# Optimization experiments

Measured on AMD Instinct MI355X. Metric: run time of the kernel, lower is better.

The kernel has to match this reference:

```python
import jax, jax.numpy as jnp
import numpy as np

D_INPUT, D_MODEL, D_OUTPUT, D_STATE, FACTOR = 100, 256, 100, 64, 2
N2 = D_STATE // 2  # complex conjugate-pair states (S4D)
B_SZ, L_SEQ = 16, 4096


def setup_inputs() -> dict:
    key = jax.random.key(0)
    ks = jax.random.split(key, 12)
    H, N = D_MODEL, N2
    # S4D ('diag-lin', zoh, real_transform='exp') parameters
    log_dt = jax.random.uniform(ks[0], (H,)) * (np.log(0.1) - np.log(0.001)) + np.log(0.001)
    log_A_real = jnp.log(0.5 * jnp.ones((H, N), jnp.float32))
    A_imag = jnp.pi * jnp.broadcast_to(jnp.arange(N, dtype=jnp.float32), (H, N))
    B_re = jnp.ones((H, N), jnp.float32)
    B_im = jnp.zeros((H, N), jnp.float32)
    C_re = jax.random.normal(ks[1], (H, N), jnp.float32)
    C_im = jax.random.normal(ks[2], (H, N), jnp.float32)
    Dskip = jax.random.normal(ks[3], (H,), jnp.float32)
    return {
        'x': jax.random.normal(ks[4], (B_SZ, L_SEQ, D_INPUT), jnp.float32),
        'enc_w': jax.random.normal(ks[5], (D_MODEL, D_INPUT), jnp.float32) / np.sqrt(D_INPUT),
        'enc_b': jnp.zeros((D_MODEL,), jnp.float32),
        'log_dt': log_dt, 'log_A_real': log_A_real, 'A_imag': A_imag,
        'B_re': B_re, 'B_im': B_im, 'C_re': C_re, 'C_im': C_im, 'Dskip': Dskip,
        'ln_g': jnp.ones((D_MODEL,), jnp.float32),
        'ln_b': jnp.zeros((D_MODEL,), jnp.float32),
        'dec1_w': jax.random.normal(ks[6], (D_MODEL * FACTOR, D_MODEL), jnp.float32) / np.sqrt(D_MODEL),
        'dec1_b': jnp.zeros((D_MODEL * FACTOR,), jnp.float32),
        'dec2_w': jax.random.normal(ks[7], (D_OUTPUT, D_MODEL * FACTOR), jnp.float32) / np.sqrt(D_MODEL * FACTOR),
        'dec2_b': jnp.zeros((D_OUTPUT,), jnp.float32),
    }


def s4d_kernel(log_dt, log_A_real, A_imag, B_re, B_im, C_re, C_im, L):
    # diagonal SSM kernel, ZOH discretization: K[h,l] = 2 Re sum_n C'_hn exp(dt_h A_hn)^l
    dt = jnp.exp(log_dt)[:, None]                      # (H,1)
    A = -jnp.exp(log_A_real) + 1j * A_imag             # (H,N)
    C = (B_re + 1j * B_im) * (C_re + 1j * C_im)        # (H,N), B folded into C
    dtA = dt * A                                       # (H,N)
    C = C * (jnp.exp(dtA) - 1.0) / A                   # ZOH correction
    V = jnp.exp(dtA[:, :, None] * jnp.arange(L))       # (H,N,L) Vandermonde
    return 2.0 * jnp.einsum('hn,hnl->hl', C, V).real   # (H,L)


def reference(x, enc_w, enc_b, log_dt, log_A_real, A_imag, B_re, B_im, C_re, C_im,
              Dskip, ln_g, ln_b, dec1_w, dec1_b, dec2_w, dec2_b):
    B, L, _ = x.shape
    u = (x @ enc_w.T + enc_b).transpose(0, 2, 1)       # (B,H,L)
    # FFTConv (single layer), dropout = identity (eval)
    k = s4d_kernel(log_dt, log_A_real, A_imag, B_re, B_im, C_re, C_im, L)
    n = 2 * L
    y = jnp.fft.irfft(jnp.fft.rfft(u, n=n) * jnp.fft.rfft(k, n=n)[None], n=n)[..., :L]
    y = y + u * Dskip[None, :, None]
    y = jax.nn.gelu(y, approximate=False)
    h = y + u                                          # residual
    # LayerNorm over channel dim
    t = h.transpose(0, 2, 1)                           # (B,L,H)
    mu = t.mean(-1, keepdims=True)
    var = jnp.mean((t - mu) ** 2, axis=-1, keepdims=True)
    t = (t - mu) / jnp.sqrt(var + 1e-5) * ln_g + ln_b
    # decoder MLP
    out = jax.nn.gelu(t @ dec1_w.T + dec1_b, approximate=False) @ dec2_w.T + dec2_b
    return out
```

## Files before the change

kernel.cpp:

```cpp
#include <hip/hip_runtime.h>
#include <hip/hip_bf16.h>

#define BB    16
#define LL    4096
#define DIN   100
#define HD    256
#define NN    32
#define DHID  512
#define DOUT  100
#define MROWS (BB*LL)
#define CH    64
#define CC    64
#define NCH   (BB*CC)

#define OFF_WRE    0
#define OFF_WIM    8192
#define OFF_KRE    16384
#define OFF_KIM    24576
#define OFF_WCHR   32768
#define OFF_WCHI   40960
#define OFF_ENCB   49152
#define OFF_DSK    49408
#define OFF_LNG    49664
#define OFF_LNB    49920
#define OFF_B1     50176
#define OFF_B2     50688
#define OFF_WENCB  50816
#define OFF_W1B    67200
#define OFF_W2B    132736
#define OFF_WFL    165504
#define OFF_BY     1230464
#define OFF_VST    2279040
#define OFF_UH     2803328
#define OFF_S      11191936
#define OFF_YH     19580544
#define OFF_TB     OFF_S
#define OFF_XB     OFF_YH

typedef __bf16 bf16x8 __attribute__((ext_vector_type(8)));
typedef float  f32x4  __attribute__((ext_vector_type(4)));

static __device__ __forceinline__ int probe_bf16(const void* lng) {
    return ((const unsigned int*)lng)[0] != 0x3f800000u;
}
static __device__ __forceinline__ float ldin(const void* p, long i, int isbf) {
    return isbf ? __bfloat162float(((const __hip_bfloat16*)p)[i]) : ((const float*)p)[i];
}
static __device__ __forceinline__ unsigned short f2bf(float v) {
    union { float f; unsigned u; } c; c.f = v;
    unsigned r = c.u + 0x7fffu + ((c.u >> 16) & 1u);
    return (unsigned short)(r >> 16);
}
static __device__ __forceinline__ float bf2f(unsigned short v) {
    union { unsigned u; float f; } c; c.u = ((unsigned)v) << 16; return c.f;
}
static __device__ __forceinline__ float gelu_f(float x) {
    float z  = fabsf(x) * 0.70710678118654752f;
    float tt = __builtin_amdgcn_rcpf(fmaf(0.3275911f, z, 1.0f));
    float p  = tt * fmaf(tt, fmaf(tt, fmaf(tt, fmaf(tt, 1.061405429f, -1.453152027f),
                          1.421413741f), -0.284496736f), 0.254829592f);
    float er = 1.0f - p * __expf(-z * z);
    return 0.5f * x * (1.0f + copysignf(er, x));
}
static __device__ __forceinline__ void gl2lds16(const unsigned short* g, unsigned short* l) {
    __builtin_amdgcn_global_load_lds(
        (const __attribute__((address_space(1))) unsigned int*)g,
        (__attribute__((address_space(3))) unsigned int*)l, 16, 0, 0);
}

__global__ __launch_bounds__(256) void k_prep(
    const void* encw, const void* encb, const void* logdt, const void* loga,
    const void* aim, const void* bre, const void* bim, const void* cre,
    const void* cim, const void* dsk, const void* lng, const void* lnb,
    const void* w1, const void* b1, const void* w2, const void* b2, float* ws)
{
    const int isbf = probe_bf16(lng);
    unsigned short* WEB = (unsigned short*)(ws + OFF_WENCB);
    unsigned short* W1B = (unsigned short*)(ws + OFF_W1B);
    unsigned short* W2B = (unsigned short*)(ws + OFF_W2B);
    const int total = 8192 + 256*4 + 512 + 128 + 32768 + 131072 + 65536;
    for (int idx = blockIdx.x * blockDim.x + threadIdx.x; idx < total;
         idx += gridDim.x * blockDim.x) {
        int i = idx;
        if (i < 8192) {
            int h = i >> 5;
            float dt  = expf(ldin(logdt, h, isbf));
            float Are = -expf(ldin(loga, i, isbf));
            float Aim = ldin(aim, i, isbf);
            float er  = expf(dt * Are);
            float sv, cv; sincosf(dt * Aim, &sv, &cv);
            float wre = er * cv, wim = er * sv;
            float Bre = ldin(bre, i, isbf), Bim = ldin(bim, i, isbf);
            float Cre = ldin(cre, i, isbf), Cim = ldin(cim, i, isbf);
            float C0re = Bre*Cre - Bim*Cim;
            float C0im = Bre*Cim + Bim*Cre;
            float inv = 1.0f / (Are*Are + Aim*Aim);
            float nre = wre - 1.0f, nim = wim;
            float Zre = (nre*Are + nim*Aim) * inv;
            float Zim = (nim*Are - nre*Aim) * inv;
            float kre = 2.0f * (C0re*Zre - C0im*Zim);
            float kim = -2.0f * (C0re*Zim + C0im*Zre);
            ws[OFF_WRE + i] = wre;  ws[OFF_WIM + i] = wim;
            ws[OFF_KRE + i] = kre;  ws[OFF_KIM + i] = kim;
            float* Wf = ws + OFF_WFL + (long)h * 4160 + 2*(i & 31);
            float pr = 1.0f, pi = 0.0f;
            for (int d = 0; d <= 64; ++d) {
                Wf[d*64]     = pr;
                Wf[d*64 + 1] = pi;
                float tr = pr*wre - pi*wim;
                pi = pr*wim + pi*wre; pr = tr;
            }
            ws[OFF_WCHR + i] = Wf[64*64];
            ws[OFF_WCHI + i] = Wf[64*64 + 1];
        } else if ((i -= 8192) < 256) {
            ws[OFF_ENCB + i] = ldin(encb, i, isbf);
        } else if ((i -= 256) < 256) {
            ws[OFF_DSK + i] = ldin(dsk, i, isbf);
        } else if ((i -= 256) < 256) {
            ws[OFF_LNG + i] = ldin(lng, i, isbf);
        } else if ((i -= 256) < 256) {
            ws[OFF_LNB + i] = ldin(lnb, i, isbf);
        } else if ((i -= 256) < 512) {
            ws[OFF_B1 + i] = ldin(b1, i, isbf);
        } else if ((i -= 512) < 128) {
            ws[OFF_B2 + i] = (i < 100) ? ldin(b2, i, isbf) : 0.0f;
        } else if ((i -= 128) < 32768) {
            int h = i >> 7, k = i & 127;
            WEB[i] = (k < 100) ? f2bf(ldin(encw, (long)h*100 + k, isbf)) : (unsigned short)0;
        } else if ((i -= 32768) < 131072) {
            W1B[i] = f2bf(ldin(w1, i, isbf));
        } else if ((i -= 131072) < 65536) {
            int j = i >> 9, k = i & 511;
            W2B[i] = (j < 100) ? f2bf(ldin(w2, (long)j*512 + k, isbf)) : (unsigned short)0;
        }
    }
}

__global__ __launch_bounds__(256) void k_xcvt(const void* x, const void* lng, float* ws)
{
    const int isbf = probe_bf16(lng);
    unsigned short* Xb = (unsigned short*)(ws + OFF_XB);
    const int total = 65536 * 16;
    for (int s = blockIdx.x * 256 + threadIdx.x; s < total; s += 1024 * 256) {
        int row = s >> 4, slot = s & 15;
        int k0 = slot * 8;
        unsigned short pk[8];
        if (!isbf) {
            const float* xr = (const float*)x + (long)row * 100;
            if (slot < 12) {
                float4 a = *(const float4*)(xr + k0);
                float4 b = *(const float4*)(xr + k0 + 4);
                pk[0]=f2bf(a.x); pk[1]=f2bf(a.y); pk[2]=f2bf(a.z); pk[3]=f2bf(a.w);
                pk[4]=f2bf(b.x); pk[5]=f2bf(b.y); pk[6]=f2bf(b.z); pk[7]=f2bf(b.w);
            } else if (slot == 12) {
                float4 a = *(const float4*)(xr + 96);
                pk[0]=f2bf(a.x); pk[1]=f2bf(a.y); pk[2]=f2bf(a.z); pk[3]=f2bf(a.w);
                pk[4]=0; pk[5]=0; pk[6]=0; pk[7]=0;
            } else {
                #pragma unroll
                for (int j = 0; j < 8; ++j) pk[j] = 0;
            }
        } else {
            const unsigned short* xr = (const unsigned short*)x + (long)row * 100;
            if (slot < 12) {
                *(uint2*)&pk[0] = *(const uint2*)(xr + k0);
                *(uint2*)&pk[4] = *(const uint2*)(xr + k0 + 4);
            } else if (slot == 12) {
                *(uint2*)&pk[0] = *(const uint2*)(xr + 96);
                pk[4]=0; pk[5]=0; pk[6]=0; pk[7]=0;
            } else {
                #pragma unroll
                for (int j = 0; j < 8; ++j) pk[j] = 0;
            }
        }
        *(float4*)&Xb[(long)row * 128 + k0] = *(const float4*)pk;
    }
}

__global__ __launch_bounds__(256) void k_tker(float* ws)
{
    __shared__ float Wp[65*65];
    __shared__ float kr[32], ki[32], Ks[64];
    int h = blockIdx.x;
    int t = threadIdx.x;
    for (int idx = t; idx < 4160; idx += 256) {
        int d = idx >> 6, c = idx & 63;
        Wp[d*65 + c] = ws[OFF_WFL + (long)h*4160 + idx];
    }
    if (t < 32) kr[t] = ws[OFF_KRE + h*32 + t];
    else if (t < 64) ki[t-32] = ws[OFF_KIM + h*32 + (t-32)];
    __syncthreads();
    if (t < 64) {
        float s = 0.0f;
        #pragma unroll
        for (int n = 0; n < 32; ++n)
            s += kr[n]*Wp[t*65 + 2*n] + ki[n]*Wp[t*65 + 2*n + 1];
        Ks[t] = s;
    }
    __syncthreads();
    unsigned short* BY = (unsigned short*)(ws + OFF_BY) + (long)h*8192;
    for (int idx = t; idx < 8192; idx += 256) {
        int j = idx >> 7, k = idx & 127;
        float v;
        if (k < 64) {
            v = (k <= j) ? Ks[j - k] : 0.0f;
        } else {
            int c = k - 64, n = c >> 1;
            float pr = Wp[(j+1)*65 + 2*n], pi = Wp[(j+1)*65 + 2*n + 1];
            v = ((c & 1) == 0) ? (kr[n]*pr + ki[n]*pi) : (ki[n]*pr - kr[n]*pi);
        }
        BY[idx] = f2bf(v);
    }
    unsigned short* Vst = (unsigned short*)(ws + OFF_VST) + (long)h*4096;
    for (int idx = t; idx < 4096; idx += 256) {
        int comp = idx >> 6, i = idx & 63;
        Vst[idx] = f2bf(Wp[(63 - i)*65 + comp]);
    }
}

__global__ __launch_bounds__(256) void k_encm(float* ws)
{
    __shared__ unsigned short SM[32768];
    unsigned short* Cs = SM;
    const unsigned short* Xb  = (const unsigned short*)(ws + OFF_XB);
    const unsigned short* WEB = (const unsigned short*)(ws + OFF_WENCB);
    int bid = blockIdx.x;
    int rt = bid >> 1, ct = bid & 1;
    long row0 = (long)rt * 128;
    int c0 = ct * 128;
    int t = threadIdx.x;
    int lane = t & 63, wv = t >> 6;
    int wm = (wv & 1) * 64, wn = (wv >> 1) * 64;
    int quad = lane >> 4, mr = lane & 15;
    int swz = lane & 7;
    int sr = t >> 3, sdst = (t & 7) * 8, ssrc = ((t & 7) ^ (sr & 7)) * 8;
    f32x4 acc[4][4] = {};
    #pragma unroll
    for (int it = 0; it < 4; ++it) {
        int r = sr + it * 32;
        gl2lds16(&Xb[(row0 + r) * 128 + ssrc], &SM[r * 64 + sdst]);
        gl2lds16(&WEB[(long)(c0 + r) * 128 + ssrc], &SM[8192 + r * 64 + sdst]);
    }
    __syncthreads();
    #pragma unroll
    for (int kc = 0; kc < 2; ++kc) {
        const unsigned short* As = &SM[(kc & 1) * 16384];
        const unsigned short* Bs = As + 8192;
        if (kc == 0) {
            #pragma unroll
            for (int it = 0; it < 4; ++it) {
                int r = sr + it * 32;
                gl2lds16(&Xb[(row0 + r) * 128 + 64 + ssrc], &SM[16384 + r * 64 + sdst]);
                gl2lds16(&WEB[(long)(c0 + r) * 128 + 64 + ssrc], &SM[24576 + r * 64 + sdst]);
            }
        }
        #pragma unroll
        for (int ks = 0; ks < 64; ks += 32) {
            int co = (((ks >> 3) | quad) ^ swz) * 8;
            bf16x8 af[4], bfr[4];
            #pragma unroll
            for (int i = 0; i < 4; ++i)
                af[i] = *(const bf16x8*)&As[(wm + i*16 + mr)*64 + co];
            #pragma unroll
            for (int j = 0; j < 4; ++j)
                bfr[j] = *(const bf16x8*)&Bs[(wn + j*16 + mr)*64 + co];
            #pragma unroll
            for (int i = 0; i < 4; ++i)
                #pragma unroll
                for (int j = 0; j < 4; ++j)
                    acc[i][j] = __builtin_amdgcn_mfma_f32_16x16x32_bf16(af[i], bfr[j], acc[i][j], 0, 0, 0);
        }
        __syncthreads();
    }
    const float* eb = ws + OFF_ENCB;
    #pragma unroll
    for (int j = 0; j < 4; ++j) {
        int hloc = wn + j*16 + mr;
        float bb = eb[c0 + hloc];
        #pragma unroll
        for (int i = 0; i < 4; ++i) {
            int l0 = wm + i*16 + quad*4;
            unsigned short pk[4];
            #pragma unroll
            for (int reg = 0; reg < 4; ++reg)
                pk[reg] = f2bf(acc[i][j][reg] + bb);
            *(uint2*)&Cs[hloc*136 + l0] = *(uint2*)pk;
        }
    }
    __syncthreads();
    unsigned short* Uh = (unsigned short*)(ws + OFF_UH);
    #pragma unroll
    for (int it = 0; it < 8; ++it) {
        int idx = t + it*256;
        int hh = idx >> 4, f = idx & 15;
        *(float4*)&Uh[(long)(c0 + hh)*65536 + row0 + f*8] = *(const float4*)&Cs[hh*136 + f*8];
    }
}

__global__ __launch_bounds__(256) void k_state(float* ws)
{
    __shared__ unsigned short As[128][72];
    __shared__ unsigned short Bs[64][72];
    const unsigned short* Uh  = (const unsigned short*)(ws + OFF_UH);
    const unsigned short* Vst = (const unsigned short*)(ws + OFF_VST);
    int bid = blockIdx.x;
    int h = bid >> 3, ct = bid & 7;
    int c0r = ct * 128;
    int t = threadIdx.x;
    int lane = t & 63, wv = t >> 6;
    int wm = (wv & 1) * 64, wn = (wv >> 1) * 32;
    int quad = lane >> 4, mr = lane & 15;
    const unsigned short* Ubase = Uh + (long)h * 65536;
    #pragma unroll
    for (int it = 0; it < 4; ++it) {
        int idx = t + it*256;
        int r = idx >> 3, f = idx & 7;
        *(float4*)&As[r][f*8] = *(const float4*)&Ubase[(long)(c0r + r)*64 + f*8];
    }
    #pragma unroll
    for (int it = 0; it < 2; ++it) {
        int idx = t + it*256;
        int r = idx >> 3, f = idx & 7;
        *(float4*)&Bs[r][f*8] = *(const float4*)&Vst[(long)h*4096 + r*64 + f*8];
    }
    __syncthreads();
    f32x4 acc[4][2] = {};
    #pragma unroll
    for (int ks = 0; ks < 64; ks += 32) {
        bf16x8 af[4], bfr[2];
        #pragma unroll
        for (int i = 0; i < 4; ++i)
            af[i] = *(const bf16x8*)&As[wm + i*16 + mr][ks + quad*8];
        #pragma unroll
        for (int jn = 0; jn < 2; ++jn)
            bfr[jn] = *(const bf16x8*)&Bs[wn + jn*16 + mr][ks + quad*8];
        #pragma unroll
        for (int i = 0; i < 4; ++i)
            #pragma unroll
            for (int jn = 0; jn < 2; ++jn)
                acc[i][jn] = __builtin_amdgcn_mfma_f32_16x16x32_bf16(af[i], bfr[jn], acc[i][jn], 0, 0, 0);
    }
    __syncthreads();
    unsigned short* Cs = &As[0][0];
    #pragma unroll
    for (int jn = 0; jn < 2; ++jn) {
        int c = wn + jn*16 + mr;
        #pragma unroll
        for (int i = 0; i < 4; ++i)
            #pragma unroll
            for (int reg = 0; reg < 4; ++reg)
                Cs[(wm + i*16 + quad*4 + reg)*72 + c] = f2bf(acc[i][jn][reg]);
    }
    __syncthreads();
    unsigned short* S = (unsigned short*)(ws + OFF_S);
    #pragma unroll
    for (int it = 0; it < 4; ++it) {
        int idx = t + it*256;
        int r = idx >> 3, f = idx & 7;
        *(float4*)&S[(long)(c0r + r)*16384 + h*64 + f*8] = *(const float4*)&Cs[r*72 + f*8];
    }
}

__global__ __launch_bounds__(256) void k_chunk(float* ws)
{
    int tid = blockIdx.x * 256 + threadIdx.x;
    int b = tid >> 13;
    int h = (tid >> 5) & 255;
    int n = tid & 31;
    int i = h * NN + n;
    float wr = ws[OFF_WCHR + i], wi = ws[OFF_WCHI + i];
    unsigned int* Su = (unsigned int*)(ws + OFF_S);
    long a0 = (long)(b * CC) * 8192 + h * 32 + n;
    float rr = 0.0f, ri = 0.0f;
    unsigned int vnext = Su[a0];
    for (int c = 0; c < CC; ++c) {
        long a = a0 + (long)c * 8192;
        unsigned int v = vnext;
        if (c + 1 < CC) vnext = Su[a + 8192];
        float Sr = bf2f((unsigned short)(v & 0xFFFFu));
        float Si = bf2f((unsigned short)(v >> 16));
        Su[a] = (unsigned int)f2bf(rr) | ((unsigned int)f2bf(ri) << 16);
        float nr = fmaf(wr, rr, fmaf(-wi, ri, Sr));
        float ni = fmaf(wr, ri, fmaf(wi, rr, Si));
        rr = nr; ri = ni;
    }
}

__global__ __launch_bounds__(256) void k_y(float* ws)
{
    __shared__ unsigned short As[128][136];
    __shared__ unsigned short Bs[64][136];
    const unsigned short* Uh = (const unsigned short*)(ws + OFF_UH);
    const unsigned short* S  = (const unsigned short*)(ws + OFF_S);
    const unsigned short* BY = (const unsigned short*)(ws + OFF_BY);
    int bid = blockIdx.x;
    int h = bid >> 3, ct = bid & 7;
    int c0r = ct * 128;
    int t = threadIdx.x;
    int lane = t & 63, wv = t >> 6;
    int wm = (wv & 1) * 64, wn = (wv >> 1) * 32;
    int quad = lane >> 4, mr = lane & 15;
    #pragma unroll
    for (int it = 0; it < 8; ++it) {
        int idx = t + it*256;
        int r = idx >> 4, f = idx & 15;
        const unsigned short* src = (f < 8)
            ? &Uh[(long)h*65536 + (long)(c0r + r)*64 + f*8]
            : &S[(long)(c0r + r)*16384 + h*64 + (f-8)*8];
        *(float4*)&As[r][f*8] = *(const float4*)src;
    }
    #pragma unroll
    for (int it = 0; it < 4; ++it) {
        int idx = t + it*256;
        int r = idx >> 4, f = idx & 15;
        *(float4*)&Bs[r][f*8] = *(const float4*)&BY[(long)h*8192 + r*128 + f*8];
    }
    __syncthreads();
    f32x4 acc[4][2] = {};
    #pragma unroll
    for (int ks = 0; ks < 128; ks += 32) {
        bf16x8 af[4], bfr[2];
        #pragma unroll
        for (int i = 0; i < 4; ++i)
            af[i] = *(const bf16x8*)&As[wm + i*16 + mr][ks + quad*8];
        #pragma unroll
        for (int jn = 0; jn < 2; ++jn)
            bfr[jn] = *(const bf16x8*)&Bs[wn + jn*16 + mr][ks + quad*8];
        #pragma unroll
        for (int i = 0; i < 4; ++i)
            #pragma unroll
            for (int jn = 0; jn < 2; ++jn)
                acc[i][jn] = __builtin_amdgcn_mfma_f32_16x16x32_bf16(af[i], bfr[jn], acc[i][jn], 0, 0, 0);
    }
    __syncthreads();
    unsigned short* Cs = &As[0][0];
    #pragma unroll
    for (int jn = 0; jn < 2; ++jn) {
        int c = wn + jn*16 + mr;
        #pragma unroll
        for (int i = 0; i < 4; ++i)
            #pragma unroll
            for (int reg = 0; reg < 4; ++reg)
                Cs[(wm + i*16 + quad*4 + reg)*136 + c] = f2bf(acc[i][jn][reg]);
    }
    __syncthreads();
    unsigned short* Yh = (unsigned short*)(ws + OFF_YH);
    #pragma unroll
    for (int it = 0; it < 4; ++it) {
        int idx = t + it*256;
        int r = idx >> 3, f = idx & 7;
        *(float4*)&Yh[(long)h*65536 + (long)(c0r + r)*64 + f*8] = *(const float4*)&Cs[r*136 + f*8];
    }
}

__global__ __launch_bounds__(1024) void k_ln2(float* ws)
{
    __shared__ unsigned short Vs[64][258];
    __shared__ float parts[64][17], partq[64][17];
    __shared__ float Ms[64], Rs[64];
    __shared__ float Dls[256], Gls[256], Bls[256];
    int chunk = blockIdx.x;
    int t = threadIdx.x;
    if (t < 256) { Dls[t] = ws[OFF_DSK + t]; Gls[t] = ws[OFF_LNG + t]; Bls[t] = ws[OFF_LNB + t]; }
    __syncthreads();
    const unsigned short* Uh = (const unsigned short*)(ws + OFF_UH);
    const unsigned short* Yh = (const unsigned short*)(ws + OFF_YH);
    int j = t & 63, hg = t >> 6;
    float ps = 0.0f, pq = 0.0f;
    #pragma unroll 4
    for (int k = 0; k < 16; ++k) {
        int h = hg*16 + k;
        long base = (long)h*65536 + chunk*64;
        float u = bf2f(Uh[base + j]);
        float y = bf2f(Yh[base + j]);
        float v = gelu_f(fmaf(Dls[h], u, y)) + u;
        Vs[j][h] = f2bf(v);
        ps += v; pq += v*v;
    }
    parts[j][hg] = ps; partq[j][hg] = pq;
    __syncthreads();
    if (t < 64) {
        float s = 0.0f, q = 0.0f;
        #pragma unroll
        for (int g = 0; g < 16; ++g) { s += parts[t][g]; q += partq[t][g]; }
        float mean = s * (1.0f/256.0f);
        float var  = q * (1.0f/256.0f) - mean*mean;
        Ms[t] = mean; Rs[t] = rsqrtf(var + 1e-5f);
    }
    __syncthreads();
    unsigned short* Tb = (unsigned short*)(ws + OFF_TB);
    int h2 = t & 255, jg = t >> 8;
    #pragma unroll 4
    for (int jj = 0; jj < 16; ++jj) {
        int j2 = jg*16 + jj;
        float v = bf2f(Vs[j2][h2]);
        Tb[((long)chunk*64 + j2)*256 + h2] = f2bf((v - Ms[j2]) * Rs[j2] * Gls[h2] + Bls[h2]);
    }
}

__global__ __launch_bounds__(256, 2) void k_dec(float* ws, void* out, const void* lng)
{
    const int isbf = probe_bf16(lng);
    __shared__ unsigned short SM[33792];
    unsigned short* Gs = SM + 16384;
    unsigned short* Cs = SM;
    const unsigned short* Tb  = (const unsigned short*)(ws + OFF_TB);
    const unsigned short* W1B = (const unsigned short*)(ws + OFF_W1B);
    const unsigned short* W2B = (const unsigned short*)(ws + OFF_W2B);
    long row0 = (long)blockIdx.x * 128;
    int t = threadIdx.x;
    int lane = t & 63, wv = t >> 6;
    int wm = (wv & 1) * 64, wn = (wv >> 1) * 64;
    int quad = lane >> 4, mr = lane & 15;
    int swz = lane & 7;
    int sr = t >> 3, sdst = (t & 7) * 8, ssrc = ((t & 7) ^ (sr & 7)) * 8;
    const float* b1 = ws + OFF_B1;
    f32x4 acc2[4][4] = {};
    #pragma unroll
    for (int it = 0; it < 4; ++it) {
        int r = sr + it * 32;
        gl2lds16(&Tb[(row0 + r) * 256 + ssrc], &SM[r * 64 + sdst]);
        gl2lds16(&W1B[(long)r * 256 + ssrc], &SM[8192 + r * 64 + sdst]);
    }
    __syncthreads();
    for (int nt = 0; nt < 4; ++nt) {
        int c0 = nt * 128;
        f32x4 acc1[4][4] = {};
        #pragma unroll
        for (int kc = 0; kc < 4; ++kc) {
            const unsigned short* As = &SM[(kc & 1) * 16384];
            const unsigned short* Bs = As + 8192;
            if (kc < 3) {
                int k0 = (kc + 1) * 64;
                unsigned short* Dst = &SM[((kc + 1) & 1) * 16384];
                #pragma unroll
                for (int it = 0; it < 4; ++it) {
                    int r = sr + it * 32;
                    gl2lds16(&Tb[(row0 + r) * 256 + k0 + ssrc], &Dst[r * 64 + sdst]);
                    gl2lds16(&W1B[(long)(c0 + r) * 256 + k0 + ssrc], &Dst[8192 + r * 64 + sdst]);
                }
            }
            #pragma unroll
            for (int ks = 0; ks < 64; ks += 32) {
                int co = (((ks >> 3) | quad) ^ swz) * 8;
                bf16x8 af[4], bfr[4];
                #pragma unroll
                for (int i = 0; i < 4; ++i)
                    af[i] = *(const bf16x8*)&As[(wm + i*16 + mr)*64 + co];
                #pragma unroll
                for (int j = 0; j < 4; ++j)
                    bfr[j] = *(const bf16x8*)&Bs[(wn + j*16 + mr)*64 + co];
                #pragma unroll
                for (int i = 0; i < 4; ++i)
                    #pragma unroll
                    for (int j = 0; j < 4; ++j)
                        acc1[i][j] = __builtin_amdgcn_mfma_f32_16x16x32_bf16(af[i], bfr[j], acc1[i][j], 0, 0, 0);
            }
            __syncthreads();
        }
        #pragma unroll
        for (int j = 0; j < 4; ++j) {
            int cloc = wn + j*16 + mr;
            float bb = b1[c0 + cloc];
            #pragma unroll
            for (int i = 0; i < 4; ++i)
                #pragma unroll
                for (int reg = 0; reg < 4; ++reg)
                    Gs[(wm + i*16 + quad*4 + reg)*136 + cloc] = f2bf(gelu_f(acc1[i][j][reg] + bb));
        }
        __syncthreads();
        if (nt < 3) {
            int c0n = c0 + 128;
            #pragma unroll
            for (int it = 0; it < 4; ++it) {
                int r = sr + it * 32;
                gl2lds16(&Tb[(row0 + r) * 256 + ssrc], &SM[r * 64 + sdst]);
                gl2lds16(&W1B[(long)(c0n + r) * 256 + ssrc], &SM[8192 + r * 64 + sdst]);
            }
        }
        #pragma unroll
        for (int ks2 = 0; ks2 < 128; ks2 += 32) {
            bf16x8 af[4], bfr[4];
            #pragma unroll
            for (int i = 0; i < 4; ++i)
                af[i] = *(const bf16x8*)&Gs[(wm + i*16 + mr)*136 + ks2 + quad*8];
            #pragma unroll
            for (int j = 0; j < 4; ++j)
                bfr[j] = *(const bf16x8*)&W2B[(long)(wn + j*16 + mr)*512 + c0 + ks2 + quad*8];
            #pragma unroll
            for (int i = 0; i < 4; ++i)
                #pragma unroll
                for (int j = 0; j < 4; ++j)
                    acc2[i][j] = __builtin_amdgcn_mfma_f32_16x16x32_bf16(af[i], bfr[j], acc2[i][j], 0, 0, 0);
        }
        __syncthreads();
    }
    const float* b2 = ws + OFF_B2;
    if (isbf) {
        #pragma unroll
        for (int j = 0; j < 4; ++j) {
            int cloc = wn + j*16 + mr;
            float bb = b2[cloc];
            #pragma unroll
            for (int i = 0; i < 4; ++i)
                #pragma unroll
                for (int reg = 0; reg < 4; ++reg)
                    Cs[(wm + i*16 + quad*4 + reg)*136 + cloc] = f2bf(acc2[i][j][reg] + bb);
        }
        __syncthreads();
        for (int idx = t; idx < 128*25; idx += 256) {
            int r = idx / 25, f = idx % 25;
            uint2* dst = (uint2*)((char*)out + (row0 + r)*200);
            dst[f] = *(const uint2*)&Cs[r*136 + f*4];
        }
    } else {
        #pragma unroll
        for (int j = 0; j < 4; ++j) {
            int col = wn + j*16 + mr;
            if (col < 100) {
                float bb = b2[col];
                #pragma unroll
                for (int i = 0; i < 4; ++i)
                    #pragma unroll
                    for (int reg = 0; reg < 4; ++reg) {
                        long row = row0 + wm + i*16 + quad*4 + reg;
                        ((float*)out)[row * 100 + col] = acc2[i][j][reg] + bb;
                    }
            }
        }
    }
}

extern "C" void kernel_launch(void* const* d_in, const int* in_sizes, int n_in,
                              void* d_out, int out_size, void* d_ws, size_t ws_size,
                              hipStream_t stream)
{
    float* ws = (float*)d_ws;
    k_prep<<<512, 256, 0, stream>>>(d_in[1], d_in[2], d_in[3], d_in[4], d_in[5],
                                    d_in[6], d_in[7], d_in[8], d_in[9], d_in[10],
                                    d_in[11], d_in[12], d_in[13], d_in[14],
                                    d_in[15], d_in[16], ws);
    k_xcvt<<<1024, 256, 0, stream>>>(d_in[0], d_in[11], ws);
    k_tker<<<256, 256, 0, stream>>>(ws);
    k_encm<<<1024, 256, 0, stream>>>(ws);
    k_state<<<2048, 256, 0, stream>>>(ws);
    k_chunk<<<512, 256, 0, stream>>>(ws);
    k_y<<<2048, 256, 0, stream>>>(ws);
    k_ln2<<<NCH, 1024, 0, stream>>>(ws);
    k_dec<<<512, 256, 0, stream>>>(ws, d_out, d_in[11]);
}
```

Measured before the change: 288.5 us.

## Restructure decoder GEMM: smaller row tiles, full-K LDS activations, direct W1 global loads

The decoder MLP kernel now processes 64 rows per block instead of 128, loading the whole 64x256 activation tile into LDS once and reading W1 fragments directly from global memory rather than double-buffering W1 chunks through LDS. This removes per-chunk barriers and LDS staging for weights, reduces shared memory, and raises occupancy (launch bounds 3, twice as many blocks). In exchange, W1 reuse per block halves, so the weights are read from global/L2 more often, and the weight loads are no longer staged asynchronously.

```diff
diff --git a/kernel.cpp b/kernel.cpp
--- a/kernel.cpp
+++ b/kernel.cpp
@@ -498,117 +498,93 @@
     }
 }
 
-__global__ __launch_bounds__(256, 2) void k_dec(float* ws, void* out, const void* lng)
+__global__ __launch_bounds__(256, 3) void k_dec(float* ws, void* out, const void* lng)
 {
     const int isbf = probe_bf16(lng);
-    __shared__ unsigned short SM[33792];
+    __shared__ unsigned short SM[25088];
     unsigned short* Gs = SM + 16384;
-    unsigned short* Cs = SM;
     const unsigned short* Tb  = (const unsigned short*)(ws + OFF_TB);
     const unsigned short* W1B = (const unsigned short*)(ws + OFF_W1B);
     const unsigned short* W2B = (const unsigned short*)(ws + OFF_W2B);
-    long row0 = (long)blockIdx.x * 128;
+    long row0 = (long)blockIdx.x * 64;
     int t = threadIdx.x;
     int lane = t & 63, wv = t >> 6;
-    int wm = (wv & 1) * 64, wn = (wv >> 1) * 64;
+    int wm = (wv & 1) * 32, wn = (wv >> 1) * 64;
     int quad = lane >> 4, mr = lane & 15;
     int swz = lane & 7;
-    int sr = t >> 3, sdst = (t & 7) * 8, ssrc = ((t & 7) ^ (sr & 7)) * 8;
     const float* b1 = ws + OFF_B1;
-    f32x4 acc2[4][4] = {};
-    #pragma unroll
-    for (int it = 0; it < 4; ++it) {
-        int r = sr + it * 32;
-        gl2lds16(&Tb[(row0 + r) * 256 + ssrc], &SM[r * 64 + sdst]);
-        gl2lds16(&W1B[(long)r * 256 + ssrc], &SM[8192 + r * 64 + sdst]);
+    f32x4 acc2[2][4] = {};
+    #pragma unroll
+    for (int it = 0; it < 8; ++it) {
+        int idx = t + it * 256;
+        int r = idx >> 5, c = idx & 31;
+        int srcc = c ^ (r & 7);
+        gl2lds16(&Tb[(row0 + r) * 256 + srcc * 8], &SM[idx * 8]);
     }
     __syncthreads();
     for (int nt = 0; nt < 4; ++nt) {
         int c0 = nt * 128;
-        f32x4 acc1[4][4] = {};
-        #pragma unroll
-        for (int kc = 0; kc < 4; ++kc) {
-            const unsigned short* As = &SM[(kc & 1) * 16384];
-            const unsigned short* Bs = As + 8192;
-            if (kc < 3) {
-                int k0 = (kc + 1) * 64;
-                unsigned short* Dst = &SM[((kc + 1) & 1) * 16384];
-                #pragma unroll
-                for (int it = 0; it < 4; ++it) {
-                    int r = sr + it * 32;
-                    gl2lds16(&Tb[(row0 + r) * 256 + k0 + ssrc], &Dst[r * 64 + sdst]);
-                    gl2lds16(&W1B[(long)(c0 + r) * 256 + k0 + ssrc], &Dst[8192 + r * 64 + sdst]);
-                }
-            }
-            #pragma unroll
-            for (int ks = 0; ks < 64; ks += 32) {
-                int co = (((ks >> 3) | quad) ^ swz) * 8;
-                bf16x8 af[4], bfr[4];
-                #pragma unroll
-                for (int i = 0; i < 4; ++i)
-                    af[i] = *(const bf16x8*)&As[(wm + i*16 + mr)*64 + co];
+        f32x4 acc1[2][4] = {};
+        #pragma unroll
+        for (int ks = 0; ks < 256; ks += 32) {
+            int co = (((ks >> 3) | quad) ^ swz) * 8;
+            bf16x8 af[2], bfr[4];
+            #pragma unroll
+            for (int i = 0; i < 2; ++i)
+                af[i] = *(const bf16x8*)&SM[(wm + i*16 + mr)*256 + co];
+            #pragma unroll
+            for (int j = 0; j < 4; ++j)
+                bfr[j] = *(const bf16x8*)&W1B[(long)(c0 + wn + j*16 + mr)*256 + ks + quad*8];
+            #pragma unroll
+            for (int i = 0; i < 2; ++i)
                 #pragma unroll
                 for (int j = 0; j < 4; ++j)
-                    bfr[j] = *(const bf16x8*)&Bs[(wn + j*16 + mr)*64 + co];
-                #pragma unroll
-                for (int i = 0; i < 4; ++i)
-                    #pragma unroll
-                    for (int j = 0; j < 4; ++j)
-                        acc1[i][j] = __builtin_amdgcn_mfma_f32_16x16x32_bf16(af[i], bfr[j], acc1[i][j], 0, 0, 0);
-            }
-            __syncthreads();
-        }
+                    acc1[i][j] = __builtin_amdgcn_mfma_f32_16x16x32_bf16(af[i], bfr[j], acc1[i][j], 0, 0, 0);
+        }
+        __syncthreads();
         #pragma unroll
         for (int j = 0; j < 4; ++j) {
             int cloc = wn + j*16 + mr;
             float bb = b1[c0 + cloc];
             #pragma unroll
-            for (int i = 0; i < 4; ++i)
+            for (int i = 0; i < 2; ++i)
                 #pragma unroll
                 for (int reg = 0; reg < 4; ++reg)
                     Gs[(wm + i*16 + quad*4 + reg)*136 + cloc] = f2bf(gelu_f(acc1[i][j][reg] + bb));
         }
         __syncthreads();
-        if (nt < 3) {
-            int c0n = c0 + 128;
-            #pragma unroll
-            for (int it = 0; it < 4; ++it) {
-                int r = sr + it * 32;
-                gl2lds16(&Tb[(row0 + r) * 256 + ssrc], &SM[r * 64 + sdst]);
-                gl2lds16(&W1B[(long)(c0n + r) * 256 + ssrc], &SM[8192 + r * 64 + sdst]);
-            }
-        }
         #pragma unroll
         for (int ks2 = 0; ks2 < 128; ks2 += 32) {
-            bf16x8 af[4], bfr[4];
-            #pragma unroll
-            for (int i = 0; i < 4; ++i)
+            bf16x8 af[2], bfr[4];
+            #pragma unroll
+            for (int i = 0; i < 2; ++i)
                 af[i] = *(const bf16x8*)&Gs[(wm + i*16 + mr)*136 + ks2 + quad*8];
             #pragma unroll
             for (int j = 0; j < 4; ++j)
                 bfr[j] = *(const bf16x8*)&W2B[(long)(wn + j*16 + mr)*512 + c0 + ks2 + quad*8];
             #pragma unroll
-            for (int i = 0; i < 4; ++i)
+            for (int i = 0; i < 2; ++i)
                 #pragma unroll
                 for (int j = 0; j < 4; ++j)
                     acc2[i][j] = __builtin_amdgcn_mfma_f32_16x16x32_bf16(af[i], bfr[j], acc2[i][j], 0, 0, 0);
         }
-        __syncthreads();
-    }
+    }
+    __syncthreads();
     const float* b2 = ws + OFF_B2;
     if (isbf) {
+        unsigned short* Cs = Gs;
         #pragma unroll
         for (int j = 0; j < 4; ++j) {
             int cloc = wn + j*16 + mr;
             float bb = b2[cloc];
             #pragma unroll
-            for (int i = 0; i < 4; ++i)
+            for (int i = 0; i < 2; ++i)
                 #pragma unroll
                 for (int reg = 0; reg < 4; ++reg)
                     Cs[(wm + i*16 + quad*4 + reg)*136 + cloc] = f2bf(acc2[i][j][reg] + bb);
         }
         __syncthreads();
-        for (int idx = t; idx < 128*25; idx += 256) {
+        for (int idx = t; idx < 64*25; idx += 256) {
             int r = idx / 25, f = idx % 25;
             uint2* dst = (uint2*)((char*)out + (row0 + r)*200);
             dst[f] = *(const uint2*)&Cs[r*136 + f*4];
@@ -620,7 +596,7 @@
             if (col < 100) {
                 float bb = b2[col];
                 #pragma unroll
-                for (int i = 0; i < 4; ++i)
+                for (int i = 0; i < 2; ++i)
                     #pragma unroll
                     for (int reg = 0; reg < 4; ++reg) {
                         long row = row0 + wm + i*16 + quad*4 + reg;
@@ -647,5 +623,5 @@
     k_chunk<<<512, 256, 0, stream>>>(ws);
     k_y<<<2048, 256, 0, stream>>>(ws);
     k_ln2<<<NCH, 1024, 0, stream>>>(ws);
-    k_dec<<<512, 256, 0, stream>>>(ws, d_out, d_in[11]);
-}
+    k_dec<<<1024, 256, 0, stream>>>(ws, d_out, d_in[11]);
+}
```

New measurement: 362.5 us. 25.6% more time.
